# Performance work log

Hardware: AMD Instinct MI355X
Metric: run time of the kernel (lower is better)

Reference implementation:

```python
import jax, jax.numpy as jnp
import numpy as np

N, D, C, S = 100000, 512, 4096, 50000


def setup_inputs() -> dict:
    key = jax.random.key(0)
    k1, k2 = jax.random.split(key)
    X = jax.random.normal(k1, (N, D), dtype=jnp.float32)
    codebook_sum = jax.random.normal(k2, (C, D), dtype=jnp.float32)
    prompt_mask = jnp.arange(N) < S  # first S rows are support (True), rest are queries
    return {"X": X, "codebook_sum": codebook_sum, "prompt_mask": prompt_mask, "num_support": S}


def reference(X, codebook_sum, prompt_mask, num_support):
    # num_support is a static Python int (replaces torch.nonzero(prompt_mask) dynamic split)
    s = num_support
    support = X[:s]                                   # [S, D] support (prompt_mask==True)
    query = X[s:]                                     # [Q, D] queries (prompt_mask==False)
    # dense similarity matmul + top-1 nearest-codebook search + gather
    cos_sim = jnp.einsum('sd,cd->sc', support, codebook_sum)  # [S, C]
    top_idx = jnp.argmax(cos_sim, axis=1)             # [S]
    code_n = codebook_sum[top_idx]                    # [S, D] gathered nearest codes
    # mean-pooled prototypes broadcast over queries
    proto = jnp.mean(support, axis=0)                 # [D]
    proto_code = jnp.mean(code_n, axis=0)             # [D]
    # euclidean distances to each prototype
    query_score = jnp.sqrt(jnp.sum((query - proto) ** 2, axis=1))        # [Q]
    query_score_code = jnp.sqrt(jnp.sum((query - proto_code) ** 2, axis=1))  # [Q]
    return (query_score + query_score_code) / 2
```

## Files before the change

kernel.cpp:

```cpp
#include <hip/hip_runtime.h>
#include <hip/hip_bf16.h>

#define NTOT 100000
#define DIM  512
#define CB   4096
#define SSUP 50000
#define NQ   (NTOT - SSUP)

#define MTILES 391
#define MPAD   (MTILES * 128)
#define NTILES 32

typedef __bf16 bf16x8 __attribute__((ext_vector_type(8)));
typedef __bf16 bf16x4 __attribute__((ext_vector_type(4)));
typedef float  f32x4  __attribute__((ext_vector_type(4)));

#define OFF_CBBF   0
#define OFF_XB     4194304
#define OFF_PV     55443456
#define OFF_PI     61849600
#define OFF_PSUM   68255744
#define OFF_PCSUM  68257792
#define OFF_HIST   68259840
#define OFF_TIDX   68276224
#define WS_NEED    (68276224 + 200000)
#define ZERO_BYTES (2048 + 2048 + 16384)

#define F_OFF_PSUM   4194304
#define F_OFF_PCSUM  4196352
#define F_OFF_HIST   4198400
#define F_OFF_TIDX   4214784

__device__ __forceinline__ void load_lds16(const void* g, void* l) {
    __builtin_amdgcn_global_load_lds(
        (const __attribute__((address_space(1))) void*)g,
        (__attribute__((address_space(3))) void*)l, 16, 0, 0);
}

__global__ void k_convert(const float* __restrict__ src, __bf16* __restrict__ dst) {
    int i = (blockIdx.x * 256 + threadIdx.x) * 4;
    float4 v = *(const float4*)(src + i);
    bf16x4 o;
    o[0] = (__bf16)v.x; o[1] = (__bf16)v.y; o[2] = (__bf16)v.z; o[3] = (__bf16)v.w;
    *(bf16x4*)(dst + i) = o;
}

__global__ void k_proto_sum(const float* __restrict__ X, float* __restrict__ protoSum) {
    const int d = threadIdx.x;
    const int r0 = blockIdx.x * 500;
    float acc = 0.f;
    for (int r = r0; r < r0 + 500; ++r)
        acc += X[(size_t)r * DIM + d];
    atomicAdd(&protoSum[d], acc);
}

__global__ __launch_bounds__(256)
void k_gemm_tile(const __bf16* __restrict__ Xb, const __bf16* __restrict__ cbb,
                 float* __restrict__ pv, int* __restrict__ pi)
{
    __shared__ __bf16 lA[128 * 32];
    __shared__ __bf16 lB[128 * 32];
    __shared__ float  sv[128][2];
    __shared__ int    si[128][2];

    const int tid  = threadIdx.x;
    const int wave = tid >> 6;
    const int lane = tid & 63;
    const int wm   = wave >> 1;
    const int wn   = wave & 1;
    const int l15  = lane & 15;
    const int q    = lane >> 4;
    const int nt   = blockIdx.x;
    const int mt   = blockIdx.y;
    const size_t r0 = (size_t)mt * 128;
    const int    c0 = nt * 128;

    f32x4 acc[4][4];
    #pragma unroll
    for (int i = 0; i < 4; ++i)
        #pragma unroll
        for (int j = 0; j < 4; ++j)
            acc[i][j] = (f32x4){0.f, 0.f, 0.f, 0.f};

    for (int k0 = 0; k0 < 512; k0 += 32) {
        __syncthreads();
        #pragma unroll
        for (int i = 0; i < 2; ++i) {
            const int ck  = i * 256 + tid;
            const int row = ck >> 2;
            const int kc  = ck & 3;
            load_lds16(Xb  + (r0 + row) * DIM + k0 + kc * 8, lA + ck * 8);
            load_lds16(cbb + (size_t)(c0 + row) * DIM + k0 + kc * 8, lB + ck * 8);
        }
        __syncthreads();

        bf16x8 af[4], bfr[4];
        #pragma unroll
        for (int t = 0; t < 4; ++t) {
            af[t]  = *(const bf16x8*)(lA + (wm * 64 + t * 16 + l15) * 32 + q * 8);
            bfr[t] = *(const bf16x8*)(lB + (wn * 64 + t * 16 + l15) * 32 + q * 8);
        }
        #pragma unroll
        for (int tm = 0; tm < 4; ++tm)
            #pragma unroll
            for (int tn = 0; tn < 4; ++tn)
                acc[tm][tn] = __builtin_amdgcn_mfma_f32_16x16x32_bf16(
                    af[tm], bfr[tn], acc[tm][tn], 0, 0, 0);
    }

    #pragma unroll
    for (int tm = 0; tm < 4; ++tm) {
        #pragma unroll
        for (int reg = 0; reg < 4; ++reg) {
            float v = -3.0e38f; int idx = 0;
            #pragma unroll
            for (int tn = 0; tn < 4; ++tn) {
                float x = acc[tm][tn][reg];
                int   c = c0 + wn * 64 + tn * 16 + l15;
                if (x > v) { v = x; idx = c; }
            }
            #pragma unroll
            for (int off = 1; off < 16; off <<= 1) {
                float ov = __shfl_xor(v, off, 64);
                int   oi = __shfl_xor(idx, off, 64);
                if (ov > v) { v = ov; idx = oi; }
            }
            if (l15 == 0) {
                int rl = wm * 64 + tm * 16 + q * 4 + reg;
                sv[rl][wn] = v;
                si[rl][wn] = idx;
            }
        }
    }
    __syncthreads();
    if (tid < 128) {
        float v0 = sv[tid][0], v1 = sv[tid][1];
        size_t r = r0 + tid;
        pv[r * 32 + nt] = fmaxf(v0, v1);
        pi[r * 32 + nt] = (v1 > v0) ? si[tid][1] : si[tid][0];
    }
}

__global__ void k_argmax_reduce(const float* __restrict__ pv, const int* __restrict__ pi,
                                int* __restrict__ top_idx) {
    int r = blockIdx.x * 256 + threadIdx.x;
    if (r >= SSUP) return;
    float v = -3.0e38f; int idx = 0;
    #pragma unroll 8
    for (int j = 0; j < 32; ++j) {
        float x = pv[(size_t)r * 32 + j];
        if (x > v) { v = x; idx = pi[(size_t)r * 32 + j]; }
    }
    top_idx[r] = idx;
}

__global__ __launch_bounds__(256, 2)
void k_gemm_argmax(const float* __restrict__ X, const __bf16* __restrict__ cbb,
                   int* __restrict__ top_idx)
{
    __shared__ float redv[64][2];
    __shared__ int   redi[64][2];

    const int tid  = threadIdx.x;
    const int wave = tid >> 6;
    const int lane = tid & 63;
    const int wm   = wave >> 1;
    const int wn   = wave & 1;
    const int l15  = lane & 15;
    const int q    = lane >> 4;
    const int r0   = blockIdx.x * 64;

    bf16x8 aflat[2][16];
    #pragma unroll
    for (int tm = 0; tm < 2; ++tm) {
        const int r = r0 + wm * 32 + tm * 16 + l15;
        const bool valid = (r < SSUP);
        const float* xr = X + (size_t)r * DIM + q * 8;
        #pragma unroll
        for (int kt = 0; kt < 16; ++kt) {
            float4 v0, v1;
            if (valid) {
                v0 = *(const float4*)(xr + kt * 32);
                v1 = *(const float4*)(xr + kt * 32 + 4);
            } else {
                v0 = make_float4(0.f, 0.f, 0.f, 0.f);
                v1 = v0;
            }
            bf16x8 f;
            f[0] = (__bf16)v0.x; f[1] = (__bf16)v0.y; f[2] = (__bf16)v0.z; f[3] = (__bf16)v0.w;
            f[4] = (__bf16)v1.x; f[5] = (__bf16)v1.y; f[6] = (__bf16)v1.z; f[7] = (__bf16)v1.w;
            aflat[tm][kt] = f;
        }
    }

    float mx[8];
    int   mi[8];
    #pragma unroll
    for (int i = 0; i < 8; ++i) { mx[i] = -3.0e38f; mi[i] = 0; }
    const f32x4 zero4 = {0.f, 0.f, 0.f, 0.f};

    for (int ct = 0; ct < 32; ++ct) {
        const int c0 = ct * 128 + wn * 64;
        const __bf16* bptr[4];
        #pragma unroll
        for (int tn = 0; tn < 4; ++tn)
            bptr[tn] = cbb + (size_t)(c0 + tn * 16 + l15) * DIM + q * 8;

        f32x4 acc[2][4];
        #pragma unroll
        for (int i = 0; i < 2; ++i)
            #pragma unroll
            for (int j = 0; j < 4; ++j)
                acc[i][j] = zero4;

        #pragma unroll
        for (int kt = 0; kt < 16; ++kt) {
            bf16x8 b[4];
            #pragma unroll
            for (int tn = 0; tn < 4; ++tn)
                b[tn] = *(const bf16x8*)(bptr[tn] + kt * 32);
            #pragma unroll
            for (int tm = 0; tm < 2; ++tm)
                #pragma unroll
                for (int tn = 0; tn < 4; ++tn)
                    acc[tm][tn] = __builtin_amdgcn_mfma_f32_16x16x32_bf16(
                        aflat[tm][kt], b[tn], acc[tm][tn], 0, 0, 0);
        }
        #pragma unroll
        for (int tm = 0; tm < 2; ++tm)
            #pragma unroll
            for (int tn = 0; tn < 4; ++tn)
                #pragma unroll
                for (int reg = 0; reg < 4; ++reg) {
                    float v = acc[tm][tn][reg];
                    int slot = tm * 4 + reg;
                    int col  = c0 + tn * 16 + l15;
                    if (v > mx[slot]) { mx[slot] = v; mi[slot] = col; }
                }
    }

    #pragma unroll
    for (int slot = 0; slot < 8; ++slot) {
        float v  = mx[slot];
        int  idx = mi[slot];
        #pragma unroll
        for (int off = 1; off < 16; off <<= 1) {
            float ov = __shfl_xor(v, off, 64);
            int   oi = __shfl_xor(idx, off, 64);
            if (ov > v) { v = ov; idx = oi; }
        }
        if (l15 == 0) {
            int rowl = wm * 32 + (slot >> 2) * 16 + q * 4 + (slot & 3);
            redv[rowl][wn] = v;
            redi[rowl][wn] = idx;
        }
    }
    __syncthreads();
    if (tid < 64) {
        int r = r0 + tid;
        if (r < SSUP) {
            float v0 = redv[tid][0], v1 = redv[tid][1];
            top_idx[r] = (v1 > v0) ? redi[tid][1] : redi[tid][0];
        }
    }
}

__global__ void k_hist(const int* __restrict__ top_idx, int* __restrict__ hist) {
    __shared__ int lh[CB];
    for (int i = threadIdx.x; i < CB; i += blockDim.x) lh[i] = 0;
    __syncthreads();
    for (int i = blockIdx.x * blockDim.x + threadIdx.x; i < SSUP; i += gridDim.x * blockDim.x)
        atomicAdd(&lh[top_idx[i]], 1);
    __syncthreads();
    for (int i = threadIdx.x; i < CB; i += blockDim.x) {
        int v = lh[i];
        if (v) atomicAdd(&hist[i], v);
    }
}

__global__ void k_proto_code(const float* __restrict__ cb, const int* __restrict__ hist,
                             float* __restrict__ pcSum) {
    const int d  = threadIdx.x;
    const int c0 = blockIdx.x * 64;
    float acc = 0.f;
    for (int c = c0; c < c0 + 64; ++c) {
        float w = (float)hist[c];
        if (w != 0.f) acc += w * cb[(size_t)c * DIM + d];
    }
    atomicAdd(&pcSum[d], acc);
}

__global__ void k_query(const float* __restrict__ X, const float* __restrict__ protoSum,
                        const float* __restrict__ pcSum, float* __restrict__ out) {
    const int lane   = threadIdx.x & 63;
    const int waveId = (blockIdx.x * blockDim.x + threadIdx.x) >> 6;
    const int nwaves = (gridDim.x * blockDim.x) >> 6;
    const float invS = 1.0f / (float)SSUP;

    for (int r = waveId; r < NQ; r += nwaves) {
        const float* xr = X + (size_t)(SSUP + r) * DIM;
        float s1 = 0.f, s2 = 0.f;
        #pragma unroll
        for (int i = 0; i < 2; ++i) {
            int dd = lane * 4 + i * 256;
            float4 xq = *(const float4*)(xr + dd);
            float4 p  = *(const float4*)(protoSum + dd);
            float4 pc = *(const float4*)(pcSum + dd);
            float d0, d1, d2, d3;
            d0 = xq.x - p.x * invS; d1 = xq.y - p.y * invS;
            d2 = xq.z - p.z * invS; d3 = xq.w - p.w * invS;
            s1 += d0 * d0 + d1 * d1 + d2 * d2 + d3 * d3;
            d0 = xq.x - pc.x * invS; d1 = xq.y - pc.y * invS;
            d2 = xq.z - pc.z * invS; d3 = xq.w - pc.w * invS;
            s2 += d0 * d0 + d1 * d1 + d2 * d2 + d3 * d3;
        }
        #pragma unroll
        for (int off = 32; off > 0; off >>= 1) {
            s1 += __shfl_xor(s1, off, 64);
            s2 += __shfl_xor(s2, off, 64);
        }
        if (lane == 0)
            out[r] = 0.5f * (sqrtf(s1) + sqrtf(s2));
    }
}

extern "C" void kernel_launch(void* const* d_in, const int* in_sizes, int n_in,
                              void* d_out, int out_size, void* d_ws, size_t ws_size,
                              hipStream_t stream) {
    const float* X  = (const float*)d_in[0];
    const float* cb = (const float*)d_in[1];
    float* out = (float*)d_out;
    char* ws = (char*)d_ws;

    __bf16* cbb = (__bf16*)(ws + OFF_CBBF);

    if (ws_size >= (size_t)WS_NEED) {
        __bf16* Xb       = (__bf16*)(ws + OFF_XB);
        float*  pv       = (float*)(ws + OFF_PV);
        int*    pi       = (int*)(ws + OFF_PI);
        float*  protoSum = (float*)(ws + OFF_PSUM);
        float*  pcSum    = (float*)(ws + OFF_PCSUM);
        int*    hist     = (int*)(ws + OFF_HIST);
        int*    top_idx  = (int*)(ws + OFF_TIDX);

        hipMemsetAsync(ws + OFF_PSUM, 0, ZERO_BYTES, stream);

        k_convert<<<(CB * DIM) / 1024, 256, 0, stream>>>(cb, cbb);
        k_convert<<<(MPAD * DIM) / 1024, 256, 0, stream>>>(X, Xb);
        k_proto_sum<<<100, 512, 0, stream>>>(X, protoSum);

        dim3 grid(NTILES, MTILES);
        k_gemm_tile<<<grid, 256, 0, stream>>>(Xb, cbb, pv, pi);

        k_argmax_reduce<<<(SSUP + 255) / 256, 256, 0, stream>>>(pv, pi, top_idx);
        k_hist<<<64, 256, 0, stream>>>(top_idx, hist);
        k_proto_code<<<CB / 64, 512, 0, stream>>>(cb, hist, pcSum);
        k_query<<<1024, 256, 0, stream>>>(X, protoSum, pcSum, out);
    } else {
        float*  protoSum = (float*)(ws + F_OFF_PSUM);
        float*  pcSum    = (float*)(ws + F_OFF_PCSUM);
        int*    hist     = (int*)(ws + F_OFF_HIST);
        int*    top_idx  = (int*)(ws + F_OFF_TIDX);

        hipMemsetAsync(ws + F_OFF_PSUM, 0, ZERO_BYTES, stream);

        k_convert<<<(CB * DIM) / 1024, 256, 0, stream>>>(cb, cbb);
        k_proto_sum<<<100, 512, 0, stream>>>(X, protoSum);
        k_gemm_argmax<<<(SSUP + 63) / 64, 256, 0, stream>>>(X, cbb, top_idx);
        k_hist<<<64, 256, 0, stream>>>(top_idx, hist);
        k_proto_code<<<CB / 64, 512, 0, stream>>>(cb, hist, pcSum);
        k_query<<<1024, 256, 0, stream>>>(X, protoSum, pcSum, out);
    }
}
```

Before: 627.7 us.

## Fuse X conversion with prototype sum and argmax reduce with histogram

Merges the X-to-bf16 conversion and the support-row column sum into one pass over X, so X is read once instead of twice. The per-tile partial max/index buffers are transposed to a column-major layout, so the final reduction reads them coalesced. That reduction is fused with the codebook histogram, which drops the top_idx buffer and one kernel launch. Kernels are reordered so the fused path uses k_proto_code and k_query defined earlier; the fallback path is unchanged.

Result: slower. 666.3 us (+6.1%).

```diff
diff --git a/kernel.cpp b/kernel.cpp
--- a/kernel.cpp
+++ b/kernel.cpp
@@ -22,8 +22,7 @@
 #define OFF_PSUM   68255744
 #define OFF_PCSUM  68257792
 #define OFF_HIST   68259840
-#define OFF_TIDX   68276224
-#define WS_NEED    (68276224 + 200000)
+#define WS_NEED    (68259840 + 16384)
 #define ZERO_BYTES (2048 + 2048 + 16384)
 
 #define F_OFF_PSUM   4194304
@@ -45,13 +44,25 @@
     *(bf16x4*)(dst + i) = o;
 }
 
-__global__ void k_proto_sum(const float* __restrict__ X, float* __restrict__ protoSum) {
-    const int d = threadIdx.x;
-    const int r0 = blockIdx.x * 500;
-    float acc = 0.f;
-    for (int r = r0; r < r0 + 500; ++r)
-        acc += X[(size_t)r * DIM + d];
-    atomicAdd(&protoSum[d], acc);
+__global__ void k_prep_support(const float* __restrict__ X, __bf16* __restrict__ Xb,
+                               float* __restrict__ protoSum) {
+    const int tid   = threadIdx.x;
+    const int rhalf = tid >> 7;
+    const int c4    = (tid & 127) * 4;
+    const size_t r0 = (size_t)blockIdx.x * 128;
+    float a0 = 0.f, a1 = 0.f, a2 = 0.f, a3 = 0.f;
+    for (int i = 0; i < 64; ++i) {
+        size_t r = r0 + (size_t)i * 2 + rhalf;
+        float4 v = *(const float4*)(X + r * DIM + c4);
+        bf16x4 o;
+        o[0] = (__bf16)v.x; o[1] = (__bf16)v.y; o[2] = (__bf16)v.z; o[3] = (__bf16)v.w;
+        *(bf16x4*)(Xb + r * DIM + c4) = o;
+        if (r < SSUP) { a0 += v.x; a1 += v.y; a2 += v.z; a3 += v.w; }
+    }
+    atomicAdd(&protoSum[c4 + 0], a0);
+    atomicAdd(&protoSum[c4 + 1], a1);
+    atomicAdd(&protoSum[c4 + 2], a2);
+    atomicAdd(&protoSum[c4 + 3], a3);
 }
 
 __global__ __launch_bounds__(256)
@@ -135,23 +146,77 @@
     __syncthreads();
     if (tid < 128) {
         float v0 = sv[tid][0], v1 = sv[tid][1];
-        size_t r = r0 + tid;
-        pv[r * 32 + nt] = fmaxf(v0, v1);
-        pi[r * 32 + nt] = (v1 > v0) ? si[tid][1] : si[tid][0];
-    }
-}
-
-__global__ void k_argmax_reduce(const float* __restrict__ pv, const int* __restrict__ pi,
-                                int* __restrict__ top_idx) {
+        pv[(size_t)nt * MPAD + r0 + tid] = fmaxf(v0, v1);
+        pi[(size_t)nt * MPAD + r0 + tid] = (v1 > v0) ? si[tid][1] : si[tid][0];
+    }
+}
+
+__global__ void k_reduce_hist(const float* __restrict__ pv, const int* __restrict__ pi,
+                              int* __restrict__ hist) {
+    __shared__ int lh[CB];
+    for (int i = threadIdx.x; i < CB; i += 256) lh[i] = 0;
+    __syncthreads();
     int r = blockIdx.x * 256 + threadIdx.x;
-    if (r >= SSUP) return;
-    float v = -3.0e38f; int idx = 0;
-    #pragma unroll 8
-    for (int j = 0; j < 32; ++j) {
-        float x = pv[(size_t)r * 32 + j];
-        if (x > v) { v = x; idx = pi[(size_t)r * 32 + j]; }
-    }
-    top_idx[r] = idx;
+    if (r < SSUP) {
+        float v = -3.0e38f; int idx = 0;
+        #pragma unroll 8
+        for (int j = 0; j < 32; ++j) {
+            float x = pv[(size_t)j * MPAD + r];
+            if (x > v) { v = x; idx = pi[(size_t)j * MPAD + r]; }
+        }
+        atomicAdd(&lh[idx], 1);
+    }
+    __syncthreads();
+    for (int i = threadIdx.x; i < CB; i += 256) {
+        int v = lh[i];
+        if (v) atomicAdd(&hist[i], v);
+    }
+}
+
+__global__ void k_proto_code(const float* __restrict__ cb, const int* __restrict__ hist,
+                             float* __restrict__ pcSum) {
+    const int d  = threadIdx.x;
+    const int c0 = blockIdx.x * 64;
+    float acc = 0.f;
+    for (int c = c0; c < c0 + 64; ++c) {
+        float w = (float)hist[c];
+        if (w != 0.f) acc += w * cb[(size_t)c * DIM + d];
+    }
+    atomicAdd(&pcSum[d], acc);
+}
+
+__global__ void k_query(const float* __restrict__ X, const float* __restrict__ protoSum,
+                        const float* __restrict__ pcSum, float* __restrict__ out) {
+    const int lane   = threadIdx.x & 63;
+    const int waveId = (blockIdx.x * blockDim.x + threadIdx.x) >> 6;
+    const int nwaves = (gridDim.x * blockDim.x) >> 6;
+    const float invS = 1.0f / (float)SSUP;
+
+    for (int r = waveId; r < NQ; r += nwaves) {
+        const float* xr = X + (size_t)(SSUP + r) * DIM;
+        float s1 = 0.f, s2 = 0.f;
+        #pragma unroll
+        for (int i = 0; i < 2; ++i) {
+            int dd = lane * 4 + i * 256;
+            float4 xq = *(const float4*)(xr + dd);
+            float4 p  = *(const float4*)(protoSum + dd);
+            float4 pc = *(const float4*)(pcSum + dd);
+            float d0, d1, d2, d3;
+            d0 = xq.x - p.x * invS; d1 = xq.y - p.y * invS;
+            d2 = xq.z - p.z * invS; d3 = xq.w - p.w * invS;
+            s1 += d0 * d0 + d1 * d1 + d2 * d2 + d3 * d3;
+            d0 = xq.x - pc.x * invS; d1 = xq.y - pc.y * invS;
+            d2 = xq.z - pc.z * invS; d3 = xq.w - pc.w * invS;
+            s2 += d0 * d0 + d1 * d1 + d2 * d2 + d3 * d3;
+        }
+        #pragma unroll
+        for (int off = 32; off > 0; off >>= 1) {
+            s1 += __shfl_xor(s1, off, 64);
+            s2 += __shfl_xor(s2, off, 64);
+        }
+        if (lane == 0)
+            out[r] = 0.5f * (sqrtf(s1) + sqrtf(s2));
+    }
 }
 
 __global__ __launch_bounds__(256, 2)
@@ -193,8 +258,7 @@
         }
     }
 
-    float mx[8];
-    int   mi[8];
+    float mx[8]; int mi[8];
     #pragma unroll
     for (int i = 0; i < 8; ++i) { mx[i] = -3.0e38f; mi[i] = 0; }
     const f32x4 zero4 = {0.f, 0.f, 0.f, 0.f};
@@ -265,6 +329,15 @@
     }
 }
 
+__global__ void k_proto_sum(const float* __restrict__ X, float* __restrict__ protoSum) {
+    const int d = threadIdx.x;
+    const int r0 = blockIdx.x * 500;
+    float acc = 0.f;
+    for (int r = r0; r < r0 + 500; ++r)
+        acc += X[(size_t)r * DIM + d];
+    atomicAdd(&protoSum[d], acc);
+}
+
 __global__ void k_hist(const int* __restrict__ top_idx, int* __restrict__ hist) {
     __shared__ int lh[CB];
     for (int i = threadIdx.x; i < CB; i += blockDim.x) lh[i] = 0;
@@ -275,52 +348,6 @@
     for (int i = threadIdx.x; i < CB; i += blockDim.x) {
         int v = lh[i];
         if (v) atomicAdd(&hist[i], v);
-    }
-}
-
-__global__ void k_proto_code(const float* __restrict__ cb, const int* __restrict__ hist,
-                             float* __restrict__ pcSum) {
-    const int d  = threadIdx.x;
-    const int c0 = blockIdx.x * 64;
-    float acc = 0.f;
-    for (int c = c0; c < c0 + 64; ++c) {
-        float w = (float)hist[c];
-        if (w != 0.f) acc += w * cb[(size_t)c * DIM + d];
-    }
-    atomicAdd(&pcSum[d], acc);
-}
-
-__global__ void k_query(const float* __restrict__ X, const float* __restrict__ protoSum,
-                        const float* __restrict__ pcSum, float* __restrict__ out) {
-    const int lane   = threadIdx.x & 63;
-    const int waveId = (blockIdx.x * blockDim.x + threadIdx.x) >> 6;
-    const int nwaves = (gridDim.x * blockDim.x) >> 6;
-    const float invS = 1.0f / (float)SSUP;
-
-    for (int r = waveId; r < NQ; r += nwaves) {
-        const float* xr = X + (size_t)(SSUP + r) * DIM;
-        float s1 = 0.f, s2 = 0.f;
-        #pragma unroll
-        for (int i = 0; i < 2; ++i) {
-            int dd = lane * 4 + i * 256;
-            float4 xq = *(const float4*)(xr + dd);
-            float4 p  = *(const float4*)(protoSum + dd);
-            float4 pc = *(const float4*)(pcSum + dd);
-            float d0, d1, d2, d3;
-            d0 = xq.x - p.x * invS; d1 = xq.y - p.y * invS;
-            d2 = xq.z - p.z * invS; d3 = xq.w - p.w * invS;
-            s1 += d0 * d0 + d1 * d1 + d2 * d2 + d3 * d3;
-            d0 = xq.x - pc.x * invS; d1 = xq.y - pc.y * invS;
-            d2 = xq.z - pc.z * invS; d3 = xq.w - pc.w * invS;
-            s2 += d0 * d0 + d1 * d1 + d2 * d2 + d3 * d3;
-        }
-        #pragma unroll
-        for (int off = 32; off > 0; off >>= 1) {
-            s1 += __shfl_xor(s1, off, 64);
-            s2 += __shfl_xor(s2, off, 64);
-        }
-        if (lane == 0)
-            out[r] = 0.5f * (sqrtf(s1) + sqrtf(s2));
     }
 }
 
@@ -341,19 +368,16 @@
         float*  protoSum = (float*)(ws + OFF_PSUM);
         float*  pcSum    = (float*)(ws + OFF_PCSUM);
         int*    hist     = (int*)(ws + OFF_HIST);
-        int*    top_idx  = (int*)(ws + OFF_TIDX);
 
         hipMemsetAsync(ws + OFF_PSUM, 0, ZERO_BYTES, stream);
 
         k_convert<<<(CB * DIM) / 1024, 256, 0, stream>>>(cb, cbb);
-        k_convert<<<(MPAD * DIM) / 1024, 256, 0, stream>>>(X, Xb);
-        k_proto_sum<<<100, 512, 0, stream>>>(X, protoSum);
+        k_prep_support<<<MTILES, 256, 0, stream>>>(X, Xb, protoSum);
 
         dim3 grid(NTILES, MTILES);
         k_gemm_tile<<<grid, 256, 0, stream>>>(Xb, cbb, pv, pi);
 
-        k_argmax_reduce<<<(SSUP + 255) / 256, 256, 0, stream>>>(pv, pi, top_idx);
-        k_hist<<<64, 256, 0, stream>>>(top_idx, hist);
+        k_reduce_hist<<<(SSUP + 255) / 256, 256, 0, stream>>>(pv, pi, hist);
         k_proto_code<<<CB / 64, 512, 0, stream>>>(cb, hist, pcSum);
         k_query<<<1024, 256, 0, stream>>>(X, protoSum, pcSum, out);
     } else {
```
